# Optimization experiments

Hardware: AMD Instinct MI355X
Metric: run time of the kernel (lower is better)

## Reference

```python
import jax, jax.numpy as jnp
import numpy as np

B, N, K = 8, 2048, 64
RADII = (0.1, 0.3, 0.7)
TU = 256   # t_net_units
U = 512    # mmtsc_units
BLK = [(512, 512), (512, 256), (256, 170)]  # pce_depth=3, filters U//(i+1)
EPS = 1e-3  # keras BatchNormalization epsilon
BN_SCALE = np.float32(1.0 / np.sqrt(1.0 + EPS))  # inference BN: mean=0, var=1


def bn(x, g, b):
    return x * (g * BN_SCALE) + b


def setup_inputs():
    key = jax.random.key(0)
    ks = jax.random.split(key, 32)
    r = lambda i, sh, s=0.1: jax.random.normal(ks[i], sh, dtype=jnp.float32) * s
    inp = {
        "points": jax.random.normal(ks[0], (B, N, 3), dtype=jnp.float32),
        "noise": jax.random.uniform(ks[1], (B, N, N), dtype=jnp.float32),
        "tw": r(2, (3, TU)), "tb": r(3, (TU,)),
        "tg1": 1.0 + r(4, (TU,)), "tbt1": r(5, (TU,)),
        "td1w": r(6, (TU, TU)), "td1b": r(7, (TU,)),
        "tg2": 1.0 + r(8, (TU,)), "tbt2": r(9, (TU,)),
        "td2w": r(10, (TU, 9), 0.01), "td2b": jnp.ones((9,), jnp.float32),
        "c1w": r(11, (3 * K * 3, U)), "c1b": r(12, (U,)),
        "g1": 1.0 + r(13, (U,)), "be1": r(14, (U,)),
        "rw": r(15, (U, U)), "rb": r(16, (U,)),
    }
    for i, (ci, co) in enumerate(BLK):
        j = 17 + 4 * i
        inp[f"b{i+1}w"] = r(j, (ci, co))
        inp[f"b{i+1}b"] = r(j + 1, (co,))
        inp[f"b{i+1}g"] = 1.0 + r(j + 2, (co,))
        inp[f"b{i+1}be"] = r(j + 3, (co,))
    return inp


def reference(points, noise, tw, tb, tg1, tbt1, td1w, td1b, tg2, tbt2, td2w, td2b,
              c1w, c1b, g1, be1, rw, rb,
              b1w, b1b, b1g, b1be, b2w, b2b, b2g, b2be, b3w, b3b, b3g, b3be):
    relu = jax.nn.relu
    # ---- T-Net (dropout inactive at inference) ----
    x = relu(bn(points @ tw + tb, tg1, tbt1))       # [B,N,TU] (1x1 conv)
    x = jnp.max(x, axis=1)                          # GlobalMaxPooling1D -> [B,TU]
    x = relu(bn(x @ td1w + td1b, tg2, tbt2))        # [B,TU]
    T = (x @ td2w + td2b).reshape(-1, 3, 3)         # [B,3,3]
    pts = points @ T                                # [B,N,3]
    # ---- pairwise distances + multi-scale ball query ----
    diff = pts[:, :, None, :] - pts[:, None, :, :]  # [B,N,N,3]
    d = jax.lax.stop_gradient(jnp.sqrt(jnp.sum(diff * diff, axis=-1)))  # [B,N,N]
    bidx = jnp.arange(B)[:, None, None]
    groups = []
    for rad in RADII:
        score = jnp.where(d <= rad, noise, 0.0)     # mask * uniform
        idx = jnp.argsort(-score, axis=-1)[:, :, :K]  # descending, top-K  [B,N,K]
        groups.append(pts[bidx, idx])               # gather -> [B,N,K,3]
    feats = jnp.concatenate(groups, axis=-1).reshape(B, N, 3 * K * 3)  # [B,N,576]
    # ---- MLP stack (1x1 convs) ----
    f = relu(bn(feats @ c1w + c1b, g1, be1))        # [B,N,U]
    f = f + (f @ rw + rb)                           # residual
    for w, b_, g, be in ((b1w, b1b, b1g, b1be), (b2w, b2b, b2g, b2be), (b3w, b3b, b3g, b3be)):
        f = relu(bn(f @ w + b_, g, be))
    return jnp.max(f, axis=1)                       # [B,170]
```

## Files before the change

kernel.cpp:

```cpp
#include <hip/hip_runtime.h>
#include <hip/hip_bf16.h>


#define BN_SCALE 0.99950037468777f

typedef short short8 __attribute__((ext_vector_type(8)));
typedef float floatx4 __attribute__((ext_vector_type(4)));

#define OFF_FEATS 0
#define OFF_R1    18874368
#define OFF_W     (OFF_R1 + 16777216)
#define OFF_C1WT  (OFF_W)
#define OFF_RWT   (OFF_C1WT + 589824)
#define OFF_B1WT  (OFF_RWT + 524288)
#define OFF_B2WT  (OFF_B1WT + 524288)
#define OFF_B3WT  (OFF_B2WT + 262144)
#define OFF_PTS   (OFF_B3WT + 131072)
#define OFF_XM    (OFF_PTS + 196608)

__device__ inline short f2bf(float x) {
    __hip_bfloat16 h = __float2bfloat16(x);
    return *reinterpret_cast<short*>(&h);
}
__device__ inline float bf2f(short s) {
    return __uint_as_float(((unsigned)(unsigned short)s) << 16);
}

__device__ inline void convw_seg(const float* src, short* dst, int K, int N, int i) {
    int n = i / K, k = i - n * K;
    float v = (n < N) ? src[(size_t)k * N + n] : 0.f;
    dst[i] = f2bf(v);
}
__global__ __launch_bounds__(256)
void convw5_k(const float* c1w, const float* rw, const float* b1w,
              const float* b2w, const float* b3w,
              short* c1wT, short* rwT, short* b1wT, short* b2wT, short* b3wT) {
    int i = blockIdx.x * 256 + threadIdx.x;
    if (i < 294912)       convw_seg(c1w, c1wT, 576, 512, i);
    else if (i < 557056)  convw_seg(rw,  rwT,  512, 512, i - 294912);
    else if (i < 819200)  convw_seg(b1w, b1wT, 512, 512, i - 557056);
    else if (i < 950272)  convw_seg(b2w, b2wT, 512, 256, i - 819200);
    else                  convw_seg(b3w, b3wT, 256, 170, i - 950272);
}

__global__ __launch_bounds__(256)
void tnet1_k(const float* __restrict__ points, const float* __restrict__ tw,
             const float* __restrict__ tb, const float* __restrict__ tg1,
             const float* __restrict__ tbt1, float* __restrict__ xm) {
    const int b = blockIdx.y;
    const int u = threadIdx.x;
    const float w0 = tw[u], w1 = tw[256 + u], w2 = tw[512 + u];
    const float bi = tb[u];
    const float gs = tg1[u] * BN_SCALE, bt = tbt1[u];
    const float* pb = points + ((size_t)b * 2048 + blockIdx.x * 256) * 3;
    float m = 0.f;
    for (int nn = 0; nn < 256; nn++) {
        float p0 = pb[nn * 3], p1 = pb[nn * 3 + 1], p2 = pb[nn * 3 + 2];
        float v = p0 * w0 + p1 * w1 + p2 * w2 + bi;
        v = fmaxf(v * gs + bt, 0.f);
        m = fmaxf(m, v);
    }
    atomicMax((unsigned int*)(xm + b * 256 + u), __float_as_uint(m));
}

__global__ __launch_bounds__(256)
void tnet2_k(const float* __restrict__ points, const float* __restrict__ xm,
             const float* __restrict__ td1w, const float* __restrict__ td1b,
             const float* __restrict__ tg2, const float* __restrict__ tbt2,
             const float* __restrict__ td2w, const float* __restrict__ td2b,
             float* __restrict__ pts_out) {
    __shared__ float sx[256], sx2[256], sT[9];
    const int b = blockIdx.x;
    const int t = threadIdx.x;
    sx[t] = xm[b * 256 + t];
    __syncthreads();
    float s = td1b[t];
    for (int v = 0; v < 256; v++) s += sx[v] * td1w[v * 256 + t];
    sx2[t] = fmaxf(s * (tg2[t] * BN_SCALE) + tbt2[t], 0.f);
    __syncthreads();
    if (t < 9) {
        float s2 = td2b[t];
        for (int v = 0; v < 256; v++) s2 += sx2[v] * td2w[v * 9 + t];
        sT[t] = s2;
    }
    __syncthreads();
    for (int n = t; n < 2048; n += 256) {
        size_t idx = ((size_t)b * 2048 + n) * 3;
        float p0 = points[idx], p1 = points[idx + 1], p2 = points[idx + 2];
        pts_out[idx]     = p0 * sT[0] + p1 * sT[3] + p2 * sT[6];
        pts_out[idx + 1] = p0 * sT[1] + p1 * sT[4] + p2 * sT[7];
        pts_out[idx + 2] = p0 * sT[2] + p1 * sT[5] + p2 * sT[8];
    }
}


__device__ inline void ins_one(unsigned& llo, unsigned& lhi, unsigned vlo,
                               unsigned vhi, int upaddr, int lane) {
    unsigned long long lv = ((unsigned long long)lhi << 32) | llo;
    unsigned long long vv = ((unsigned long long)vhi << 32) | vlo;
    unsigned long long ltm = __ballot(lv < vv);
    if (ltm) {
        int p = __builtin_ctzll(ltm);
        unsigned uplo = (unsigned)__builtin_amdgcn_ds_bpermute(upaddr, (int)llo);
        unsigned uphi = (unsigned)__builtin_amdgcn_ds_bpermute(upaddr, (int)lhi);
        if (lane >= p) {
            llo = (lane == p) ? vlo : uplo;
            lhi = (lane == p) ? vhi : uphi;
        }
    }
}

__device__ inline void run_q(unsigned& llo, unsigned& lhi, unsigned long long& th,
                             unsigned klo, unsigned khi, unsigned long long qual,
                             int upaddr, int lane) {
    do {
        int src = __builtin_ctzll(qual);
        qual &= qual - 1;
        unsigned vlo = (unsigned)__builtin_amdgcn_readlane((int)klo, src);
        unsigned vhi = (unsigned)__builtin_amdgcn_readlane((int)khi, src);
        ins_one(llo, lhi, vlo, vhi, upaddr, lane);
    } while (qual);
    th = ((unsigned long long)(unsigned)__builtin_amdgcn_readlane((int)lhi, 63) << 32)
         | (unsigned)__builtin_amdgcn_readlane((int)llo, 63);
}

__device__ inline void init_radius(bool in, unsigned nb, unsigned klo, int lane,
                                   int upaddr, unsigned& llo, unsigned& lhi,
                                   unsigned long long& th) {
    unsigned long long inm = __ballot(in);
    int S = 64 - __builtin_popcountll(inm);
    int mbI = __builtin_amdgcn_mbcnt_hi((unsigned)(inm >> 32),
              __builtin_amdgcn_mbcnt_lo((unsigned)inm, 0));
    int mbS = lane - mbI;
    int dst = in ? (S + mbI) : mbS;
    llo = (unsigned)__builtin_amdgcn_ds_permute(dst << 2, in ? 0 : (int)klo);
    lhi = 0;
    if (inm) {
        do {
            int src = __builtin_ctzll(inm);
            inm &= inm - 1;
            unsigned vlo = (unsigned)__builtin_amdgcn_readlane((int)klo, src);
            unsigned vhi = (unsigned)__builtin_amdgcn_readlane((int)nb, src);
            ins_one(llo, lhi, vlo, vhi, upaddr, lane);
        } while (inm);
    }
    th = ((unsigned long long)(unsigned)__builtin_amdgcn_readlane((int)lhi, 63) << 32)
         | (unsigned)__builtin_amdgcn_readlane((int)llo, 63);
}

__global__ __launch_bounds__(1024)
void topk_feats_k(const float* __restrict__ pts, const float* __restrict__ noise,
                  short* __restrict__ feats) {
    __shared__ float sxp[2048], syp[2048], szp[2048];
    const int b = blockIdx.y;
    const int tid = threadIdx.x;
    const int lane = tid & 63;
    const int wave = tid >> 6;
    const int n = blockIdx.x * 16 + wave;
    const float* nrow = noise + ((size_t)b * 2048 + n) * 2048;
    float ncur = nrow[lane];
    float nnxt = nrow[64 + lane];
    for (int i = tid; i < 2048; i += 1024) {
        size_t p = ((size_t)b * 2048 + i) * 3;
        sxp[i] = pts[p];
        syp[i] = pts[p + 1];
        szp[i] = pts[p + 2];
    }
    __syncthreads();
    const float qx = sxp[n], qy = syp[n], qz = szp[n];
    const int upaddr = (lane - 1) << 2;

    unsigned L0lo, L0hi, L1lo, L1hi, L2lo, L2hi;
    unsigned long long th0, th1, th2;

    {
        float dx = qx - sxp[lane], dy = qy - syp[lane], dz = qz - szp[lane];
        float d = sqrtf(dx * dx + dy * dy + dz * dz);
        unsigned nb = __float_as_uint(ncur);
        unsigned klo = 2047 - lane;
        init_radius(d <= 0.1f, nb, klo, lane, upaddr, L0lo, L0hi, th0);
        init_radius(d <= 0.3f, nb, klo, lane, upaddr, L1lo, L1hi, th1);
        init_radius(d <= 0.7f, nb, klo, lane, upaddr, L2lo, L2hi, th2);
    }
    for (int base = 64; base < 2048; base += 64) {
        float cur = nnxt;
        if (base + 64 < 2048) nnxt = nrow[base + 64 + lane];
        const int j = base + lane;
        float dx = qx - sxp[j], dy = qy - syp[j], dz = qz - szp[j];
        float d = sqrtf(dx * dx + dy * dy + dz * dz);
        unsigned nb = __float_as_uint(cur);
        unsigned klo = 2047 - j;
        unsigned k0hi = (d <= 0.1f) ? nb : 0u;
        unsigned k1hi = (d <= 0.3f) ? nb : 0u;
        unsigned k2hi = (d <= 0.7f) ? nb : 0u;
        unsigned long long key0 = ((unsigned long long)k0hi << 32) | klo;
        unsigned long long key1 = ((unsigned long long)k1hi << 32) | klo;
        unsigned long long key2 = ((unsigned long long)k2hi << 32) | klo;
        unsigned long long q0 = __ballot(key0 > th0);
        unsigned long long q1 = __ballot(key1 > th1);
        unsigned long long q2 = __ballot(key2 > th2);
        if (q0) run_q(L0lo, L0hi, th0, klo, k0hi, q0, upaddr, lane);
        if (q1) run_q(L1lo, L1hi, th1, klo, k1hi, q1, upaddr, lane);
        if (q2) run_q(L2lo, L2hi, th2, klo, k2hi, q2, upaddr, lane);
    }

    size_t basef = ((size_t)b * 2048 + n) * 576 + (size_t)lane * 9;
    int j0 = 2047 - (int)(L0lo & 0x7FFu);
    int j1 = 2047 - (int)(L1lo & 0x7FFu);
    int j2 = 2047 - (int)(L2lo & 0x7FFu);
    feats[basef + 0] = f2bf(sxp[j0]);
    feats[basef + 1] = f2bf(syp[j0]);
    feats[basef + 2] = f2bf(szp[j0]);
    feats[basef + 3] = f2bf(sxp[j1]);
    feats[basef + 4] = f2bf(syp[j1]);
    feats[basef + 5] = f2bf(szp[j1]);
    feats[basef + 6] = f2bf(sxp[j2]);
    feats[basef + 7] = f2bf(syp[j2]);
    feats[basef + 8] = f2bf(szp[j2]);
}

template <int EPI>
__global__ __launch_bounds__(256)
void gemm_k(const short* __restrict__ A, const short* __restrict__ BT,
            int K, int Nact,
            const float* __restrict__ bias, const float* __restrict__ gamma,
            const float* __restrict__ beta,
            short* __restrict__ outB, float* __restrict__ outF,
            const short* __restrict__ resid) {
    __shared__ short sA[128 * 40];
    __shared__ short sB[128 * 40];
    const int tid = threadIdx.x;
    const int lane = tid & 63;
    const int wave = tid >> 6;
    const int wm = wave & 1, wn = wave >> 1;
    const int lr = lane & 15, lq = lane >> 4;
    const long m0 = (long)blockIdx.x * 128;
    const long n0 = (long)blockIdx.y * 128;

    floatx4 acc[4][4];
#pragma unroll
    for (int i = 0; i < 4; i++)
#pragma unroll
        for (int j = 0; j < 4; j++) acc[i][j] = (floatx4){0.f, 0.f, 0.f, 0.f};

    for (int k0 = 0; k0 < K; k0 += 32) {
        __syncthreads();
#pragma unroll
        for (int cc = 0; cc < 2; cc++) {
            int c = tid + cc * 256;
            int rr = c >> 2, p = (c & 3) * 8;
            *(uint4*)(&sA[rr * 40 + p]) = *(const uint4*)(A + (m0 + rr) * K + k0 + p);
            *(uint4*)(&sB[rr * 40 + p]) = *(const uint4*)(BT + (n0 + rr) * K + k0 + p);
        }
        __syncthreads();
        short8 af[4], bf[4];
#pragma unroll
        for (int i = 0; i < 4; i++)
            af[i] = *(const short8*)(&sA[(wm * 64 + i * 16 + lr) * 40 + lq * 8]);
#pragma unroll
        for (int j = 0; j < 4; j++)
            bf[j] = *(const short8*)(&sB[(wn * 64 + j * 16 + lr) * 40 + lq * 8]);
#pragma unroll
        for (int i = 0; i < 4; i++)
#pragma unroll
            for (int j = 0; j < 4; j++)
                acc[i][j] = __builtin_amdgcn_mfma_f32_16x16x32_bf16(af[i], bf[j],
                                                                    acc[i][j], 0, 0, 0);
    }

#pragma unroll
    for (int j = 0; j < 4; j++) {
        long col = n0 + wn * 64 + j * 16 + lr;
        if (col >= Nact) continue;
        float bi = bias[col];
        float gs = 0.f, bt = 0.f;
        if (EPI != 1) { gs = gamma[col] * BN_SCALE; bt = beta[col]; }
        float colmax = 0.f;
#pragma unroll
        for (int i = 0; i < 4; i++) {
#pragma unroll
            for (int rg = 0; rg < 4; rg++) {
                long row = m0 + wm * 64 + i * 16 + lq * 4 + rg;
                float v = acc[i][j][rg];
                if (EPI == 1) {
                    v = v + bi + bf2f(resid[row * Nact + col]);
                    outB[row * Nact + col] = f2bf(v);
                } else {
                    v = fmaxf((v + bi) * gs + bt, 0.f);
                    if (EPI == 0) outB[row * Nact + col] = f2bf(v);
                    else colmax = fmaxf(colmax, v);
                }
            }
        }
        if (EPI == 2) {
            colmax = fmaxf(colmax, __shfl_xor(colmax, 16));
            colmax = fmaxf(colmax, __shfl_xor(colmax, 32));
            if (lq == 0) {
                int bb = (int)(m0 >> 11);
                atomicMax((unsigned int*)&outF[bb * 170 + col],
                          __float_as_uint(colmax));
            }
        }
    }
}

extern "C" void kernel_launch(void* const* d_in, const int* in_sizes, int n_in,
                              void* d_out, int out_size, void* d_ws, size_t ws_size,
                              hipStream_t stream) {
    const float* points = (const float*)d_in[0];
    const float* noise  = (const float*)d_in[1];
    const float* tw   = (const float*)d_in[2];
    const float* tb   = (const float*)d_in[3];
    const float* tg1  = (const float*)d_in[4];
    const float* tbt1 = (const float*)d_in[5];
    const float* td1w = (const float*)d_in[6];
    const float* td1b = (const float*)d_in[7];
    const float* tg2  = (const float*)d_in[8];
    const float* tbt2 = (const float*)d_in[9];
    const float* td2w = (const float*)d_in[10];
    const float* td2b = (const float*)d_in[11];
    const float* c1w  = (const float*)d_in[12];
    const float* c1b  = (const float*)d_in[13];
    const float* g1   = (const float*)d_in[14];
    const float* be1  = (const float*)d_in[15];
    const float* rw   = (const float*)d_in[16];
    const float* rb   = (const float*)d_in[17];
    const float* b1w  = (const float*)d_in[18];
    const float* b1b  = (const float*)d_in[19];
    const float* b1g  = (const float*)d_in[20];
    const float* b1be = (const float*)d_in[21];
    const float* b2w  = (const float*)d_in[22];
    const float* b2b  = (const float*)d_in[23];
    const float* b2g  = (const float*)d_in[24];
    const float* b2be = (const float*)d_in[25];
    const float* b3w  = (const float*)d_in[26];
    const float* b3b  = (const float*)d_in[27];
    const float* b3g  = (const float*)d_in[28];
    const float* b3be = (const float*)d_in[29];

    char* ws = (char*)d_ws;
    short* feats = (short*)(ws + OFF_FEATS);
    short* f1    = (short*)(ws + OFF_R1);
    short* f2    = feats;
    short* f3    = (short*)(ws + OFF_R1);
    short* f4    = feats;
    short* c1wT  = (short*)(ws + OFF_C1WT);
    short* rwT   = (short*)(ws + OFF_RWT);
    short* b1wT  = (short*)(ws + OFF_B1WT);
    short* b2wT  = (short*)(ws + OFF_B2WT);
    short* b3wT  = (short*)(ws + OFF_B3WT);
    float* pts   = (float*)(ws + OFF_PTS);
    float* xm    = (float*)(ws + OFF_XM);

    hipMemsetAsync(xm, 0, 8 * 256 * sizeof(float), stream);
    hipMemsetAsync(d_out, 0, (size_t)out_size * sizeof(float), stream);

    convw5_k<<<3968, 256, 0, stream>>>(c1w, rw, b1w, b2w, b3w,
                                       c1wT, rwT, b1wT, b2wT, b3wT);

    tnet1_k<<<dim3(8, 8), 256, 0, stream>>>(points, tw, tb, tg1, tbt1, xm);
    tnet2_k<<<8, 256, 0, stream>>>(points, xm, td1w, td1b, tg2, tbt2, td2w, td2b, pts);
    topk_feats_k<<<dim3(128, 8), 1024, 0, stream>>>(pts, noise, feats);

    gemm_k<0><<<dim3(128, 4), 256, 0, stream>>>(feats, c1wT, 576, 512, c1b, g1, be1,
                                                f1, nullptr, nullptr);
    gemm_k<1><<<dim3(128, 4), 256, 0, stream>>>(f1, rwT, 512, 512, rb, nullptr, nullptr,
                                                f2, nullptr, f1);
    gemm_k<0><<<dim3(128, 4), 256, 0, stream>>>(f2, b1wT, 512, 512, b1b, b1g, b1be,
                                                f3, nullptr, nullptr);
    gemm_k<0><<<dim3(128, 2), 256, 0, stream>>>(f3, b2wT, 512, 256, b2b, b2g, b2be,
                                                f4, nullptr, nullptr);
    gemm_k<2><<<dim3(128, 2), 256, 0, stream>>>(f4, b3wT, 256, 170, b3b, b3g, b3be,
                                                nullptr, (float*)d_out, nullptr);
}
```

Baseline: 479.8 us.

## Fuse MLP GEMM chain into one LDS-resident kernel and tile weight transpose

Replaces five separate GEMM launches with a single kernel where each block keeps a 64-row activation tile in LDS across all layers, avoiding global round-trips of intermediate activations. The weight conversion becomes a shared-memory tiled transpose for coalesced access, and the T-Net max uses per-block partials instead of atomics plus a memset. Trade-off: one block per CU with weights read directly from global/L2 each step, lowering parallelism and possibly MFMA feed efficiency.

After: 463.1 us. 3.5% less time.

```diff
diff --git a/kernel.cpp b/kernel.cpp
--- a/kernel.cpp
+++ b/kernel.cpp
@@ -8,15 +8,14 @@
 typedef float floatx4 __attribute__((ext_vector_type(4)));
 
 #define OFF_FEATS 0
-#define OFF_R1    18874368
-#define OFF_W     (OFF_R1 + 16777216)
+#define OFF_W     18874368
 #define OFF_C1WT  (OFF_W)
 #define OFF_RWT   (OFF_C1WT + 589824)
 #define OFF_B1WT  (OFF_RWT + 524288)
 #define OFF_B2WT  (OFF_B1WT + 524288)
 #define OFF_B3WT  (OFF_B2WT + 262144)
 #define OFF_PTS   (OFF_B3WT + 131072)
-#define OFF_XM    (OFF_PTS + 196608)
+#define OFF_PART  (OFF_PTS + 196608)
 
 __device__ inline short f2bf(float x) {
     __hip_bfloat16 h = __float2bfloat16(x);
@@ -26,27 +25,42 @@
     return __uint_as_float(((unsigned)(unsigned short)s) << 16);
 }
 
-__device__ inline void convw_seg(const float* src, short* dst, int K, int N, int i) {
-    int n = i / K, k = i - n * K;
-    float v = (n < N) ? src[(size_t)k * N + n] : 0.f;
-    dst[i] = f2bf(v);
-}
 __global__ __launch_bounds__(256)
-void convw5_k(const float* c1w, const float* rw, const float* b1w,
-              const float* b2w, const float* b3w,
-              short* c1wT, short* rwT, short* b1wT, short* b2wT, short* b3wT) {
-    int i = blockIdx.x * 256 + threadIdx.x;
-    if (i < 294912)       convw_seg(c1w, c1wT, 576, 512, i);
-    else if (i < 557056)  convw_seg(rw,  rwT,  512, 512, i - 294912);
-    else if (i < 819200)  convw_seg(b1w, b1wT, 512, 512, i - 557056);
-    else if (i < 950272)  convw_seg(b2w, b2wT, 512, 256, i - 819200);
-    else                  convw_seg(b3w, b3wT, 256, 170, i - 950272);
+void convw_t_k(const float* __restrict__ c1w, const float* __restrict__ rw,
+               const float* __restrict__ b1w, const float* __restrict__ b2w,
+               const float* __restrict__ b3w,
+               short* __restrict__ c1wT, short* __restrict__ rwT,
+               short* __restrict__ b1wT, short* __restrict__ b2wT,
+               short* __restrict__ b3wT) {
+    __shared__ float tile[64][65];
+    int bid = blockIdx.x;
+    const float* src; short* dst; int K, N, t;
+    if (bid < 72)       { src = c1w; dst = c1wT; K = 576; N = 512; t = bid; }
+    else if (bid < 136) { src = rw;  dst = rwT;  K = 512; N = 512; t = bid - 72; }
+    else if (bid < 200) { src = b1w; dst = b1wT; K = 512; N = 512; t = bid - 136; }
+    else if (bid < 232) { src = b2w; dst = b2wT; K = 512; N = 256; t = bid - 200; }
+    else                { src = b3w; dst = b3wT; K = 256; N = 170; t = bid - 232; }
+    int ktiles = K >> 6;
+    int k0 = (t % ktiles) * 64, n0 = (t / ktiles) * 64;
+    int tx = threadIdx.x & 63, ty = threadIdx.x >> 6;
+#pragma unroll
+    for (int p = 0; p < 16; p++) {
+        int r = p * 4 + ty;
+        int n = n0 + tx;
+        tile[r][tx] = (n < N) ? src[(size_t)(k0 + r) * N + n] : 0.f;
+    }
+    __syncthreads();
+#pragma unroll
+    for (int p = 0; p < 16; p++) {
+        int r = p * 4 + ty;
+        dst[(size_t)(n0 + r) * K + k0 + tx] = f2bf(tile[tx][r]);
+    }
 }
 
 __global__ __launch_bounds__(256)
 void tnet1_k(const float* __restrict__ points, const float* __restrict__ tw,
              const float* __restrict__ tb, const float* __restrict__ tg1,
-             const float* __restrict__ tbt1, float* __restrict__ xm) {
+             const float* __restrict__ tbt1, float* __restrict__ part) {
     const int b = blockIdx.y;
     const int u = threadIdx.x;
     const float w0 = tw[u], w1 = tw[256 + u], w2 = tw[512 + u];
@@ -60,11 +74,11 @@
         v = fmaxf(v * gs + bt, 0.f);
         m = fmaxf(m, v);
     }
-    atomicMax((unsigned int*)(xm + b * 256 + u), __float_as_uint(m));
+    part[((b * 8 + blockIdx.x) << 8) + u] = m;
 }
 
 __global__ __launch_bounds__(256)
-void tnet2_k(const float* __restrict__ points, const float* __restrict__ xm,
+void tnet2_k(const float* __restrict__ points, const float* __restrict__ part,
              const float* __restrict__ td1w, const float* __restrict__ td1b,
              const float* __restrict__ tg2, const float* __restrict__ tbt2,
              const float* __restrict__ td2w, const float* __restrict__ td2b,
@@ -72,7 +86,10 @@
     __shared__ float sx[256], sx2[256], sT[9];
     const int b = blockIdx.x;
     const int t = threadIdx.x;
-    sx[t] = xm[b * 256 + t];
+    float m = 0.f;
+#pragma unroll
+    for (int c = 0; c < 8; c++) m = fmaxf(m, part[((b * 8 + c) << 8) + t]);
+    sx[t] = m;
     __syncthreads();
     float s = td1b[t];
     for (int v = 0; v < 256; v++) s += sx[v] * td1w[v * 256 + t];
@@ -92,7 +109,6 @@
         pts_out[idx + 2] = p0 * sT[2] + p1 * sT[5] + p2 * sT[8];
     }
 }
-
 
 __device__ inline void ins_one(unsigned& llo, unsigned& lhi, unsigned vlo,
                                unsigned vhi, int upaddr, int lane) {
@@ -172,7 +188,6 @@
 
     unsigned L0lo, L0hi, L1lo, L1hi, L2lo, L2hi;
     unsigned long long th0, th1, th2;
-
     {
         float dx = qx - sxp[lane], dy = qy - syp[lane], dz = qz - szp[lane];
         float d = sqrtf(dx * dx + dy * dy + dz * dz);
@@ -203,7 +218,6 @@
         if (q1) run_q(L1lo, L1hi, th1, klo, k1hi, q1, upaddr, lane);
         if (q2) run_q(L2lo, L2hi, th2, klo, k2hi, q2, upaddr, lane);
     }
-
     size_t basef = ((size_t)b * 2048 + n) * 576 + (size_t)lane * 9;
     int j0 = 2047 - (int)(L0lo & 0x7FFu);
     int j1 = 2047 - (int)(L1lo & 0x7FFu);
@@ -219,87 +233,156 @@
     feats[basef + 8] = f2bf(szp[j2]);
 }
 
-template <int EPI>
-__global__ __launch_bounds__(256)
-void gemm_k(const short* __restrict__ A, const short* __restrict__ BT,
-            int K, int Nact,
-            const float* __restrict__ bias, const float* __restrict__ gamma,
-            const float* __restrict__ beta,
-            short* __restrict__ outB, float* __restrict__ outF,
-            const short* __restrict__ resid) {
-    __shared__ short sA[128 * 40];
-    __shared__ short sB[128 * 40];
-    const int tid = threadIdx.x;
-    const int lane = tid & 63;
-    const int wave = tid >> 6;
-    const int wm = wave & 1, wn = wave >> 1;
-    const int lr = lane & 15, lq = lane >> 4;
-    const long m0 = (long)blockIdx.x * 128;
-    const long n0 = (long)blockIdx.y * 128;
-
-    floatx4 acc[4][4];
-#pragma unroll
-    for (int i = 0; i < 4; i++)
-#pragma unroll
-        for (int j = 0; j < 4; j++) acc[i][j] = (floatx4){0.f, 0.f, 0.f, 0.f};
-
-    for (int k0 = 0; k0 < K; k0 += 32) {
-        __syncthreads();
-#pragma unroll
-        for (int cc = 0; cc < 2; cc++) {
-            int c = tid + cc * 256;
-            int rr = c >> 2, p = (c & 3) * 8;
-            *(uint4*)(&sA[rr * 40 + p]) = *(const uint4*)(A + (m0 + rr) * K + k0 + p);
-            *(uint4*)(&sB[rr * 40 + p]) = *(const uint4*)(BT + (n0 + rr) * K + k0 + p);
+
+__device__ inline int act_addr(int r, int c) {
+    return r * 512 + ((((c >> 3) ^ (r & 7)) << 3) | (c & 7));
+}
+
+template <int KST, int JT>
+__device__ inline void mm_lds(const short* __restrict__ act,
+                              const short* __restrict__ BT, int K, int colbase,
+                              int lr, int lq, floatx4 (&acc)[4][JT]) {
+#pragma unroll 4
+    for (int ks = 0; ks < KST; ks++) {
+        short8 af[4], bf[JT];
+        int g = ks * 4 + lq;
+#pragma unroll
+        for (int i = 0; i < 4; i++) {
+            int r = i * 16 + lr;
+            af[i] = *(const short8*)(act + r * 512 + ((g ^ (lr & 7)) << 3));
         }
-        __syncthreads();
-        short8 af[4], bf[4];
+#pragma unroll
+        for (int j = 0; j < JT; j++)
+            bf[j] = *(const short8*)(BT + (size_t)(colbase + j * 16 + lr) * K +
+                                     ks * 32 + lq * 8);
 #pragma unroll
         for (int i = 0; i < 4; i++)
-            af[i] = *(const short8*)(&sA[(wm * 64 + i * 16 + lr) * 40 + lq * 8]);
-#pragma unroll
-        for (int j = 0; j < 4; j++)
-            bf[j] = *(const short8*)(&sB[(wn * 64 + j * 16 + lr) * 40 + lq * 8]);
-#pragma unroll
-        for (int i = 0; i < 4; i++)
-#pragma unroll
-            for (int j = 0; j < 4; j++)
+#pragma unroll
+            for (int j = 0; j < JT; j++)
                 acc[i][j] = __builtin_amdgcn_mfma_f32_16x16x32_bf16(af[i], bf[j],
                                                                     acc[i][j], 0, 0, 0);
     }
-
-#pragma unroll
-    for (int j = 0; j < 4; j++) {
-        long col = n0 + wn * 64 + j * 16 + lr;
-        if (col >= Nact) continue;
-        float bi = bias[col];
-        float gs = 0.f, bt = 0.f;
-        if (EPI != 1) { gs = gamma[col] * BN_SCALE; bt = beta[col]; }
-        float colmax = 0.f;
-#pragma unroll
-        for (int i = 0; i < 4; i++) {
-#pragma unroll
-            for (int rg = 0; rg < 4; rg++) {
-                long row = m0 + wm * 64 + i * 16 + lq * 4 + rg;
-                float v = acc[i][j][rg];
-                if (EPI == 1) {
-                    v = v + bi + bf2f(resid[row * Nact + col]);
-                    outB[row * Nact + col] = f2bf(v);
-                } else {
-                    v = fmaxf((v + bi) * gs + bt, 0.f);
-                    if (EPI == 0) outB[row * Nact + col] = f2bf(v);
-                    else colmax = fmaxf(colmax, v);
+}
+
+template <int JT, bool RELU, bool RESID>
+__device__ inline void epi_store(short* __restrict__ act, floatx4 (&acc)[4][JT],
+                                 int colbase, int lr, int lq,
+                                 const float* __restrict__ bias,
+                                 const float* __restrict__ gamma,
+                                 const float* __restrict__ beta) {
+    short st[4][JT][4];
+#pragma unroll
+    for (int j = 0; j < JT; j++) {
+        int c = colbase + j * 16 + lr;
+        float bi = bias[c];
+        float gs = RELU ? gamma[c] * BN_SCALE : 0.f;
+        float bt = RELU ? beta[c] : 0.f;
+#pragma unroll
+        for (int i = 0; i < 4; i++)
+#pragma unroll
+            for (int reg = 0; reg < 4; reg++) {
+                int r = i * 16 + lq * 4 + reg;
+                float v = acc[i][j][reg] + bi;
+                if (RESID) v += bf2f(act[act_addr(r, c)]);
+                if (RELU) v = fmaxf(v * gs + bt, 0.f);
+                st[i][j][reg] = f2bf(v);
+            }
+    }
+    __syncthreads();
+#pragma unroll
+    for (int j = 0; j < JT; j++) {
+        int c = colbase + j * 16 + lr;
+#pragma unroll
+        for (int i = 0; i < 4; i++)
+#pragma unroll
+            for (int reg = 0; reg < 4; reg++) {
+                int r = i * 16 + lq * 4 + reg;
+                act[act_addr(r, c)] = st[i][j][reg];
+            }
+    }
+    __syncthreads();
+}
+
+__global__ __launch_bounds__(512)
+void chain_k(const short* __restrict__ feats,
+             const short* __restrict__ c1wT, const short* __restrict__ rwT,
+             const short* __restrict__ b1wT, const short* __restrict__ b2wT,
+             const short* __restrict__ b3wT,
+             const float* __restrict__ c1b, const float* __restrict__ g1,
+             const float* __restrict__ be1, const float* __restrict__ rb,
+             const float* __restrict__ b1b, const float* __restrict__ b1g,
+             const float* __restrict__ b1be,
+             const float* __restrict__ b2b, const float* __restrict__ b2g,
+             const float* __restrict__ b2be,
+             const float* __restrict__ b3b, const float* __restrict__ b3g,
+             const float* __restrict__ b3be,
+             float* __restrict__ out) {
+    __shared__ short act[64 * 512];
+    const int tid = threadIdx.x;
+    const int lane = tid & 63, wq = tid >> 6;
+    const int lr = lane & 15, lq = lane >> 4;
+    const long m0 = (long)blockIdx.x * 64;
+
+    {
+        floatx4 acc[4][4] = {};
+        const short* Ab = feats + (m0 + lr) * 576 + lq * 8;
+        const short* Bb = c1wT + (size_t)(wq * 64 + lr) * 576 + lq * 8;
+#pragma unroll 4
+        for (int ks = 0; ks < 18; ks++) {
+            short8 af[4], bf[4];
+#pragma unroll
+            for (int i = 0; i < 4; i++)
+                af[i] = *(const short8*)(Ab + (size_t)i * 16 * 576 + ks * 32);
+#pragma unroll
+            for (int j = 0; j < 4; j++)
+                bf[j] = *(const short8*)(Bb + (size_t)j * 16 * 576 + ks * 32);
+#pragma unroll
+            for (int i = 0; i < 4; i++)
+#pragma unroll
+                for (int j = 0; j < 4; j++)
+                    acc[i][j] = __builtin_amdgcn_mfma_f32_16x16x32_bf16(
+                        af[i], bf[j], acc[i][j], 0, 0, 0);
+        }
+        epi_store<4, true, false>(act, acc, wq * 64, lr, lq, c1b, g1, be1);
+    }
+    {
+        floatx4 acc[4][4] = {};
+        mm_lds<16, 4>(act, rwT, 512, wq * 64, lr, lq, acc);
+        epi_store<4, false, true>(act, acc, wq * 64, lr, lq, rb, nullptr, nullptr);
+    }
+    {
+        floatx4 acc[4][4] = {};
+        mm_lds<16, 4>(act, b1wT, 512, wq * 64, lr, lq, acc);
+        epi_store<4, true, false>(act, acc, wq * 64, lr, lq, b1b, b1g, b1be);
+    }
+    {
+        floatx4 acc[4][2] = {};
+        mm_lds<16, 2>(act, b2wT, 512, wq * 32, lr, lq, acc);
+        epi_store<2, true, false>(act, acc, wq * 32, lr, lq, b2b, b2g, b2be);
+    }
+    {
+        floatx4 acc[4][2] = {};
+        mm_lds<8, 2>(act, b3wT, 256, wq * 32, lr, lq, acc);
+        const int bb = blockIdx.x >> 5;
+#pragma unroll
+        for (int j = 0; j < 2; j++) {
+            int c = wq * 32 + j * 16 + lr;
+            bool valid = (c < 170);
+            float bi = valid ? b3b[c] : 0.f;
+            float gs = valid ? b3g[c] * BN_SCALE : 0.f;
+            float bt = valid ? b3be[c] : 0.f;
+            float cm = 0.f;
+#pragma unroll
+            for (int i = 0; i < 4; i++)
+#pragma unroll
+                for (int reg = 0; reg < 4; reg++) {
+                    float v = fmaxf((acc[i][j][reg] + bi) * gs + bt, 0.f);
+                    cm = fmaxf(cm, v);
                 }
-            }
-        }
-        if (EPI == 2) {
-            colmax = fmaxf(colmax, __shfl_xor(colmax, 16));
-            colmax = fmaxf(colmax, __shfl_xor(colmax, 32));
-            if (lq == 0) {
-                int bb = (int)(m0 >> 11);
-                atomicMax((unsigned int*)&outF[bb * 170 + col],
-                          __float_as_uint(colmax));
-            }
+            cm = fmaxf(cm, __shfl_xor(cm, 16));
+            cm = fmaxf(cm, __shfl_xor(cm, 32));
+            if (lq == 0 && valid)
+                atomicMax((unsigned int*)&out[bb * 170 + c], __float_as_uint(cm));
         }
     }
 }
@@ -340,36 +423,24 @@
 
     char* ws = (char*)d_ws;
     short* feats = (short*)(ws + OFF_FEATS);
-    short* f1    = (short*)(ws + OFF_R1);
-    short* f2    = feats;
-    short* f3    = (short*)(ws + OFF_R1);
-    short* f4    = feats;
     short* c1wT  = (short*)(ws + OFF_C1WT);
     short* rwT   = (short*)(ws + OFF_RWT);
     short* b1wT  = (short*)(ws + OFF_B1WT);
     short* b2wT  = (short*)(ws + OFF_B2WT);
     short* b3wT  = (short*)(ws + OFF_B3WT);
     float* pts   = (float*)(ws + OFF_PTS);
-    float* xm    = (float*)(ws + OFF_XM);
-
-    hipMemsetAsync(xm, 0, 8 * 256 * sizeof(float), stream);
+    float* part  = (float*)(ws + OFF_PART);
+
     hipMemsetAsync(d_out, 0, (size_t)out_size * sizeof(float), stream);
 
-    convw5_k<<<3968, 256, 0, stream>>>(c1w, rw, b1w, b2w, b3w,
+    convw_t_k<<<248, 256, 0, stream>>>(c1w, rw, b1w, b2w, b3w,
                                        c1wT, rwT, b1wT, b2wT, b3wT);
-
-    tnet1_k<<<dim3(8, 8), 256, 0, stream>>>(points, tw, tb, tg1, tbt1, xm);
-    tnet2_k<<<8, 256, 0, stream>>>(points, xm, td1w, td1b, tg2, tbt2, td2w, td2b, pts);
+    tnet1_k<<<dim3(8, 8), 256, 0, stream>>>(points, tw, tb, tg1, tbt1, part);
+    tnet2_k<<<8, 256, 0, stream>>>(points, part, td1w, td1b, tg2, tbt2,
+                                   td2w, td2b, pts);
     topk_feats_k<<<dim3(128, 8), 1024, 0, stream>>>(pts, noise, feats);
-
-    gemm_k<0><<<dim3(128, 4), 256, 0, stream>>>(feats, c1wT, 576, 512, c1b, g1, be1,
-                                                f1, nullptr, nullptr);
-    gemm_k<1><<<dim3(128, 4), 256, 0, stream>>>(f1, rwT, 512, 512, rb, nullptr, nullptr,
-                                                f2, nullptr, f1);
-    gemm_k<0><<<dim3(128, 4), 256, 0, stream>>>(f2, b1wT, 512, 512, b1b, b1g, b1be,
-                                                f3, nullptr, nullptr);
-    gemm_k<0><<<dim3(128, 2), 256, 0, stream>>>(f3, b2wT, 512, 256, b2b, b2g, b2be,
-                                                f4, nullptr, nullptr);
-    gemm_k<2><<<dim3(128, 2), 256, 0, stream>>>(f4, b3wT, 256, 170, b3b, b3g, b3be,
-                                                nullptr, (float*)d_out, nullptr);
-}
+    chain_k<<<256, 512, 0, stream>>>(feats, c1wT, rwT, b1wT, b2wT, b3wT,
+                                     c1b, g1, be1, rb, b1b, b1g, b1be,
+                                     b2b, b2g, b2be, b3b, b3g, b3be,
+                                     (float*)d_out);
+}
```
